# Kernel optimization log

Hardware: AMD Instinct MI355X
Metric: run time of the kernel (lower is better)

## Reference

```python
import jax, jax.numpy as jnp
import numpy as np

CONF_THRESHOLD = 0.7

def setup_inputs() -> dict:
    key = jax.random.key(0)
    ks = jax.random.split(key, 8)
    B, T, D, H, GH = 16384, 48, 32, 1024, 128
    s = lambda fan: 1.0 / np.sqrt(fan)
    return {
        "x":   jax.random.normal(ks[0], (B, T, D), jnp.float32),
        "gW1": jax.random.normal(ks[1], (D, GH), jnp.float32) * s(D),
        "gb1": jnp.zeros((GH,), jnp.float32),
        "gW2": jax.random.normal(ks[2], (GH, 2), jnp.float32) * s(GH),
        "gb2": jnp.zeros((2,), jnp.float32),
        "nW1": jax.random.normal(ks[3], (T * D, H), jnp.float32) * s(T * D),
        "nb1": jnp.zeros((H,), jnp.float32),
        "nW2": jax.random.normal(ks[4], (H, 2), jnp.float32) * s(H),
        "nb2": jnp.zeros((2,), jnp.float32),
        "aW1": jax.random.normal(ks[5], (T * D, H), jnp.float32) * s(T * D),
        "ab1": jnp.zeros((H,), jnp.float32),
        "aW2": jax.random.normal(ks[6], (H, 2), jnp.float32) * s(H),
        "ab2": jnp.zeros((2,), jnp.float32),
    }

def _gate(x, gW1, gb1, gW2, gb2):
    # mean-pool over time, 2-layer MLP, softmax -> [B, 2] class probs
    h = jax.nn.relu(jnp.mean(x, axis=1) @ gW1 + gb1)
    return jax.nn.softmax(h @ gW2 + gb2, axis=-1)

def _expert(x_flat, W1, b1, W2, b2):
    return jax.nn.relu(x_flat @ W1 + b1) @ W2 + b2

def reference(x, gW1, gb1, gW2, gb2, nW1, nb1, nW2, nb2, aW1, ab1, aW2, ab2):
    B = x.shape[0]
    gate_outputs = _gate(x, gW1, gb1, gW2, gb2)          # [B, 2]
    gate_probs = jnp.max(gate_outputs, axis=1)           # [B]
    gate_decisions = jnp.argmax(gate_outputs, axis=1)    # [B] in {0,1}

    # adaptive routing: low-confidence samples fall back to the normal expert
    high_conf = gate_probs >= CONF_THRESHOLD
    abnormal_mask = high_conf & (gate_decisions == 1)
    # normal_mask = (high_conf & dec==0) | ~high_conf  == ~abnormal_mask (partition)

    x_flat = x.reshape(B, -1)
    normal_out = _expert(x_flat, nW1, nb1, nW2, nb2)     # [B, 2]
    abnormal_out = _expert(x_flat, aW1, ab1, aW2, ab2)   # [B, 2]
    outputs = jnp.where(abnormal_mask[:, None], abnormal_out, normal_out)
    return outputs, gate_decisions, gate_probs
```

## Files before the change

kernel.cpp:

```cpp
#include <hip/hip_runtime.h>

#define TDIM 48
#define DDIM 32
#define KDIM 1536
#define HDIM 1024
#define GHID 128

typedef unsigned short u16;
typedef __bf16 bf16x8 __attribute__((ext_vector_type(8)));
typedef float  f32x4  __attribute__((ext_vector_type(4)));

typedef const void __attribute__((address_space(1))) gvoid;
typedef void       __attribute__((address_space(3))) lvoid;

__device__ __forceinline__ void gld_lds16(const void* g, void* l) {
    __builtin_amdgcn_global_load_lds((gvoid*)g, (lvoid*)l, 16, 0, 0);
}

__device__ __forceinline__ u16 f2bf(float f) {
    union { float f; unsigned u; } v; v.f = f;
    return (u16)((v.u + 0x7fffu + ((v.u >> 16) & 1u)) >> 16);
}

__global__ __launch_bounds__(256) void gate_kernel(
    const float* __restrict__ x,
    const float* __restrict__ gW1, const float* __restrict__ gb1,
    const float* __restrict__ gW2, const float* __restrict__ gb2,
    u16* __restrict__ Xbf, int* __restrict__ route, int* __restrict__ cnt,
    float* __restrict__ out, float* __restrict__ outDec, float* __restrict__ outProb)
{
    const int wave = threadIdx.x >> 6;
    const int lane = threadIdx.x & 63;
    const int b    = blockIdx.x * 4 + wave;
    if (blockIdx.x == 0 && threadIdx.x < 2) cnt[threadIdx.x] = 0;

    const float* xr = x + (size_t)b * KDIM;
    u16* xo = Xbf + (size_t)b * KDIM;

    double a0 = 0, a1 = 0, a2 = 0, a3 = 0;
#pragma unroll
    for (int i = 0; i < 6; ++i) {
        const int idx = i * 256 + lane * 4;
        float4 v = *(const float4*)(xr + idx);
        ushort4 o;
        o.x = f2bf(v.x); o.y = f2bf(v.y); o.z = f2bf(v.z); o.w = f2bf(v.w);
        *(ushort4*)(xo + idx) = o;
        a0 += v.x; a1 += v.y; a2 += v.z; a3 += v.w;
    }
#pragma unroll
    for (int m = 8; m <= 32; m <<= 1) {
        a0 += __shfl_xor(a0, m); a1 += __shfl_xor(a1, m);
        a2 += __shfl_xor(a2, m); a3 += __shfl_xor(a3, m);
    }
    __shared__ double xm[4][DDIM];
    if (lane < 8) {
        xm[wave][4 * lane + 0] = a0 / 48.0; xm[wave][4 * lane + 1] = a1 / 48.0;
        xm[wave][4 * lane + 2] = a2 / 48.0; xm[wave][4 * lane + 3] = a3 / 48.0;
    }
    __builtin_amdgcn_wave_barrier();
    __builtin_amdgcn_s_waitcnt(0);
    __threadfence_block();

    double h0 = (double)gb1[lane], h1 = (double)gb1[lane + 64];
#pragma unroll
    for (int d = 0; d < DDIM; ++d) {
        const double xv = xm[wave][d];
        h0 += xv * (double)gW1[d * GHID + lane];
        h1 += xv * (double)gW1[d * GHID + 64 + lane];
    }
    h0 = h0 > 0.0 ? h0 : 0.0;
    h1 = h1 > 0.0 ? h1 : 0.0;
    double z0 = h0 * (double)gW2[lane * 2 + 0] + h1 * (double)gW2[(lane + 64) * 2 + 0];
    double z1 = h0 * (double)gW2[lane * 2 + 1] + h1 * (double)gW2[(lane + 64) * 2 + 1];
#pragma unroll
    for (int m = 1; m <= 32; m <<= 1) {
        z0 += __shfl_xor(z0, m);
        z1 += __shfl_xor(z1, m);
    }
    if (lane == 0) {
        z0 += (double)gb2[0]; z1 += (double)gb2[1];
        const int dec = (z1 > z0) ? 1 : 0;
        const double mz = z0 > z1 ? z0 : z1;
        const double e0 = exp(z0 - mz), e1 = exp(z1 - mz);
        const double p = (e0 > e1 ? e0 : e1) / (e0 + e1);
        const float pf = (float)p;
        outDec[b]  = (float)dec;
        outProb[b] = pf;
        out[2 * b + 0] = 0.f;
        out[2 * b + 1] = 0.f;
        const int high = ((double)pf >= 0.7) ? 1 : 0;
        route[b] = (high && dec) ? 1 : 0;
    }
}

__global__ __launch_bounds__(256) void transpose_cast(
    const float* __restrict__ nW1, const float* __restrict__ aW1,
    u16* __restrict__ W1t)
{
    __shared__ float tile[32][33];
    const int e  = blockIdx.z;
    const float* W = e ? aW1 : nW1;
    u16* Wt = W1t + (size_t)e * HDIM * KDIM;
    const int bx = blockIdx.x;
    const int by = blockIdx.y;
    const int tx = threadIdx.x;
    const int ty = threadIdx.y;
#pragma unroll
    for (int r = 0; r < 32; r += 8)
        tile[ty + r][tx] = W[(size_t)(by * 32 + ty + r) * HDIM + bx * 32 + tx];
    __syncthreads();
#pragma unroll
    for (int r = 0; r < 32; r += 8)
        Wt[(size_t)(bx * 32 + ty + r) * KDIM + by * 32 + tx] = f2bf(tile[tx][ty + r]);
}

__global__ __launch_bounds__(256) void compact_kernel(
    const int* __restrict__ route, int* __restrict__ perm, int* __restrict__ cnt,
    int Bn)
{
    const int b    = blockIdx.x * 256 + threadIdx.x;
    const int lane = threadIdx.x & 63;
    const int active = (b < Bn);
    const int e = active ? route[b] : 0;
    const unsigned long long m1 = __ballot(active && e == 1);
    const unsigned long long m0 = __ballot(active && e == 0);
    const unsigned long long below = (lane == 63) ? ~0ull >> 1 : ((1ull << lane) - 1);
    int base0 = 0, base1 = 0;
    if (lane == 0) {
        if (m0) base0 = atomicAdd(&cnt[0], (int)__popcll(m0));
        if (m1) base1 = atomicAdd(&cnt[1], (int)__popcll(m1));
    }
    base0 = __shfl(base0, 0);
    base1 = __shfl(base1, 0);
    if (active) {
        const int pos = e ? base1 + (int)__popcll(m1 & below)
                          : base0 + (int)__popcll(m0 & below);
        perm[e * Bn + pos] = b;
    }
}

__global__ __launch_bounds__(256, 2) void expert_gemm(
    const u16* __restrict__ Xbf, const u16* __restrict__ W1t,
    const float* __restrict__ nb1, const float* __restrict__ nW2,
    const float* __restrict__ nb2,
    const float* __restrict__ ab1, const float* __restrict__ aW2,
    const float* __restrict__ ab2,
    const int* __restrict__ perm, const int* __restrict__ cnt,
    float* __restrict__ out, int Bn, int mBlocks)
{
    __shared__ __align__(16) u16 Alds[128 * 32];
    __shared__ __align__(16) u16 Blds[128 * 32];
    __shared__ int   permLds[128];
    __shared__ float w2Lds[128 * 2];
    __shared__ float b1Lds[128];

    const int tid = threadIdx.x;
    const int f    = (int)blockIdx.x;
    const int g    = f >> 6;
    const int nIdx = (f >> 3) & 7;
    const int mGlb = g * 8 + (f & 7);
    const int e  = mGlb >= mBlocks;
    const int mb = mGlb - (e ? mBlocks : 0);
    const int cntE = cnt[e];
    const int start = mb * 128;
    if (start >= cntE) return;
    const int valid = min(128, cntE - start);

    const int n0 = nIdx * 128;
    const u16*  W1e = W1t + (size_t)e * HDIM * KDIM;
    const float* b1 = e ? ab1 : nb1;
    const float* w2 = e ? aW2 : nW2;
    const float* b2 = e ? ab2 : nb2;

    if (tid < 128) permLds[tid] = perm[e * Bn + min(start + tid, cntE - 1)];
    if (tid >= 128) {
        const int j = tid - 128;
        b1Lds[j]        = b1[n0 + j];
        w2Lds[j * 2 + 0] = w2[(n0 + j) * 2 + 0];
        w2Lds[j * 2 + 1] = w2[(n0 + j) * 2 + 1];
    }
    __syncthreads();

    const int rA0 = permLds[tid >> 2];
    const int rA1 = permLds[(tid + 256) >> 2];
    const u16* gA0 = Xbf + (size_t)rA0 * KDIM + (tid & 3) * 8;
    const u16* gA1 = Xbf + (size_t)rA1 * KDIM + (tid & 3) * 8;
    const u16* gB0 = W1e + (size_t)(n0 + (tid >> 2)) * KDIM + (tid & 3) * 8;
    const u16* gB1 = W1e + (size_t)(n0 + 64 + (tid >> 2)) * KDIM + (tid & 3) * 8;

    const int wave = tid >> 6;
    const int lane = tid & 63;
    const int wm   = (wave & 1) * 64;
    const int wn   = (wave >> 1) * 64;
    const int l15  = lane & 15;
    const int quad = lane >> 4;

    f32x4 acc[4][4];
#pragma unroll
    for (int i = 0; i < 4; ++i)
#pragma unroll
        for (int j = 0; j < 4; ++j) acc[i][j] = (f32x4)0.f;

    for (int k0 = 0; k0 < KDIM; k0 += 32) {
        gld_lds16(gA0 + k0, &Alds[tid * 8]);
        gld_lds16(gA1 + k0, &Alds[(tid + 256) * 8]);
        gld_lds16(gB0 + k0, &Blds[tid * 8]);
        gld_lds16(gB1 + k0, &Blds[(tid + 256) * 8]);
        __syncthreads();

        bf16x8 af[4], bfv[4];
#pragma unroll
        for (int mi = 0; mi < 4; ++mi)
            af[mi] = *reinterpret_cast<const bf16x8*>(&Alds[(wm + mi * 16 + l15) * 32 + quad * 8]);
#pragma unroll
        for (int ni = 0; ni < 4; ++ni)
            bfv[ni] = *reinterpret_cast<const bf16x8*>(&Blds[(wn + ni * 16 + l15) * 32 + quad * 8]);
#pragma unroll
        for (int mi = 0; mi < 4; ++mi)
#pragma unroll
            for (int ni = 0; ni < 4; ++ni)
                acc[mi][ni] = __builtin_amdgcn_mfma_f32_16x16x32_bf16(af[mi], bfv[ni], acc[mi][ni], 0, 0, 0);
        __syncthreads();
    }

    const float b2_0 = (n0 == 0) ? b2[0] : 0.f;
    const float b2_1 = (n0 == 0) ? b2[1] : 0.f;
#pragma unroll
    for (int mi = 0; mi < 4; ++mi) {
        float p0[4] = {0.f, 0.f, 0.f, 0.f};
        float p1[4] = {0.f, 0.f, 0.f, 0.f};
#pragma unroll
        for (int ni = 0; ni < 4; ++ni) {
            const int col = wn + ni * 16 + l15;
            const float w20 = w2Lds[col * 2 + 0];
            const float w21 = w2Lds[col * 2 + 1];
            const float bb  = b1Lds[col];
#pragma unroll
            for (int r = 0; r < 4; ++r) {
                float h = acc[mi][ni][r] + bb;
                h = fmaxf(h, 0.f);
                p0[r] += h * w20;
                p1[r] += h * w21;
            }
        }
#pragma unroll
        for (int m = 1; m <= 8; m <<= 1) {
#pragma unroll
            for (int r = 0; r < 4; ++r) {
                p0[r] += __shfl_xor(p0[r], m);
                p1[r] += __shfl_xor(p1[r], m);
            }
        }
        if (l15 < 4) {
            const int r = l15;
            const int lrow = wm + mi * 16 + quad * 4 + r;
            if (lrow < valid) {
                const int srow = permLds[lrow];
                atomicAdd(&out[srow * 2 + 0], p0[r] + b2_0);
                atomicAdd(&out[srow * 2 + 1], p1[r] + b2_1);
            }
        }
    }
}

extern "C" void kernel_launch(void* const* d_in, const int* in_sizes, int n_in,
                              void* d_out, int out_size, void* d_ws, size_t ws_size,
                              hipStream_t stream) {
    const float* x   = (const float*)d_in[0];
    const float* gW1 = (const float*)d_in[1];
    const float* gb1 = (const float*)d_in[2];
    const float* gW2 = (const float*)d_in[3];
    const float* gb2 = (const float*)d_in[4];
    const float* nW1 = (const float*)d_in[5];
    const float* nb1 = (const float*)d_in[6];
    const float* nW2 = (const float*)d_in[7];
    const float* nb2 = (const float*)d_in[8];
    const float* aW1 = (const float*)d_in[9];
    const float* ab1 = (const float*)d_in[10];
    const float* aW2 = (const float*)d_in[11];
    const float* ab2 = (const float*)d_in[12];

    float* out = (float*)d_out;
    const int Bn = in_sizes[0] / KDIM;

    char* ws = (char*)d_ws;
    size_t off = 0;
    u16* Xbf = (u16*)(ws + off); off += (size_t)Bn * KDIM * sizeof(u16);
    u16* W1t = (u16*)(ws + off); off += (size_t)2 * HDIM * KDIM * sizeof(u16);
    int* perm = (int*)(ws + off); off += (size_t)2 * Bn * sizeof(int);
    int* cnt  = (int*)(ws + off); off += 2 * sizeof(int);
    int* route = (int*)(ws + off); off += (size_t)Bn * sizeof(int);

    gate_kernel<<<Bn / 4, 256, 0, stream>>>(x, gW1, gb1, gW2, gb2,
                                            Xbf, route, cnt,
                                            out, out + 2 * Bn, out + 3 * Bn);

    transpose_cast<<<dim3(HDIM / 32, KDIM / 32, 2), dim3(32, 8), 0, stream>>>(nW1, aW1, W1t);

    compact_kernel<<<(Bn + 255) / 256, 256, 0, stream>>>(route, perm, cnt, Bn);

    const int mBlocks = (Bn + 127) / 128;
    expert_gemm<<<8 * 2 * mBlocks, 256, 0, stream>>>(
        Xbf, W1t, nb1, nW2, nb2, ab1, aW2, ab2, perm, cnt, out, Bn, mBlocks);
}
```

Measured before the change: 253.8 us.

## Switch expert GEMM to 32x32x16 MFMA with K=64 tiles and k-group LDS layout

Replaces the 16x16x32 MFMA tiling with 32x32x16 bf16 MFMAs, doubles the K step per iteration to 64, and reorganizes LDS as [kgroup][row][8] so each async load fills a contiguous 16-byte slot. The aim is fewer barriers per K, fewer LDS fragment reads per FLOP, and better LDS bank behavior. The launch bound is raised to 4 blocks per CU for more occupancy. The epilogue is adapted to the 32x32 accumulator layout with a wider shuffle reduction. The higher block count may cap registers per thread and cause spills.

```diff
diff --git a/kernel.cpp b/kernel.cpp
--- a/kernel.cpp
+++ b/kernel.cpp
@@ -9,6 +9,7 @@
 typedef unsigned short u16;
 typedef __bf16 bf16x8 __attribute__((ext_vector_type(8)));
 typedef float  f32x4  __attribute__((ext_vector_type(4)));
+typedef float  f32x16 __attribute__((ext_vector_type(16)));
 
 typedef const void __attribute__((address_space(1))) gvoid;
 typedef void       __attribute__((address_space(3))) lvoid;
@@ -139,7 +140,7 @@
     }
 }
 
-__global__ __launch_bounds__(256, 2) void expert_gemm(
+__global__ __launch_bounds__(256, 4) void expert_gemm(
     const u16* __restrict__ Xbf, const u16* __restrict__ W1t,
     const float* __restrict__ nb1, const float* __restrict__ nW2,
     const float* __restrict__ nb2,
@@ -148,17 +149,17 @@
     const int* __restrict__ perm, const int* __restrict__ cnt,
     float* __restrict__ out, int Bn, int mBlocks)
 {
-    __shared__ __align__(16) u16 Alds[128 * 32];
-    __shared__ __align__(16) u16 Blds[128 * 32];
+    __shared__ __align__(16) u16 Alds[8][128][8];
+    __shared__ __align__(16) u16 Blds[8][128][8];
     __shared__ int   permLds[128];
     __shared__ float w2Lds[128 * 2];
     __shared__ float b1Lds[128];
 
     const int tid = threadIdx.x;
     const int f    = (int)blockIdx.x;
-    const int g    = f >> 6;
+    const int g4   = f >> 6;
     const int nIdx = (f >> 3) & 7;
-    const int mGlb = g * 8 + (f & 7);
+    const int mGlb = g4 * 8 + (f & 7);
     const int e  = mGlb >= mBlocks;
     const int mb = mGlb - (e ? mBlocks : 0);
     const int cntE = cnt[e];
@@ -181,83 +182,87 @@
     }
     __syncthreads();
 
-    const int rA0 = permLds[tid >> 2];
-    const int rA1 = permLds[(tid + 256) >> 2];
-    const u16* gA0 = Xbf + (size_t)rA0 * KDIM + (tid & 3) * 8;
-    const u16* gA1 = Xbf + (size_t)rA1 * KDIM + (tid & 3) * 8;
-    const u16* gB0 = W1e + (size_t)(n0 + (tid >> 2)) * KDIM + (tid & 3) * 8;
-    const u16* gB1 = W1e + (size_t)(n0 + 64 + (tid >> 2)) * KDIM + (tid & 3) * 8;
+    const int rowS  = tid & 127;
+    const int gBase = tid >> 7;
+    const u16* gA = Xbf + (size_t)permLds[rowS] * KDIM + gBase * 8;
+    const u16* gB = W1e + (size_t)(n0 + rowS) * KDIM + gBase * 8;
+    u16* la = (u16*)Alds + tid * 8;
+    u16* lb = (u16*)Blds + tid * 8;
 
     const int wave = tid >> 6;
     const int lane = tid & 63;
     const int wm   = (wave & 1) * 64;
     const int wn   = (wave >> 1) * 64;
-    const int l15  = lane & 15;
-    const int quad = lane >> 4;
-
-    f32x4 acc[4][4];
-#pragma unroll
-    for (int i = 0; i < 4; ++i)
-#pragma unroll
-        for (int j = 0; j < 4; ++j) acc[i][j] = (f32x4)0.f;
-
-    for (int k0 = 0; k0 < KDIM; k0 += 32) {
-        gld_lds16(gA0 + k0, &Alds[tid * 8]);
-        gld_lds16(gA1 + k0, &Alds[(tid + 256) * 8]);
-        gld_lds16(gB0 + k0, &Blds[tid * 8]);
-        gld_lds16(gB1 + k0, &Blds[(tid + 256) * 8]);
+    const int l31  = lane & 31;
+    const int khalf = lane >> 5;
+
+    f32x16 acc00 = (f32x16)0.f, acc01 = (f32x16)0.f;
+    f32x16 acc10 = (f32x16)0.f, acc11 = (f32x16)0.f;
+
+    for (int k0 = 0; k0 < KDIM; k0 += 64) {
+#pragma unroll
+        for (int j = 0; j < 4; ++j)
+            gld_lds16(gA + k0 + j * 16, la + j * 2048);
+#pragma unroll
+        for (int j = 0; j < 4; ++j)
+            gld_lds16(gB + k0 + j * 16, lb + j * 2048);
         __syncthreads();
 
-        bf16x8 af[4], bfv[4];
-#pragma unroll
-        for (int mi = 0; mi < 4; ++mi)
-            af[mi] = *reinterpret_cast<const bf16x8*>(&Alds[(wm + mi * 16 + l15) * 32 + quad * 8]);
-#pragma unroll
-        for (int ni = 0; ni < 4; ++ni)
-            bfv[ni] = *reinterpret_cast<const bf16x8*>(&Blds[(wn + ni * 16 + l15) * 32 + quad * 8]);
-#pragma unroll
-        for (int mi = 0; mi < 4; ++mi)
-#pragma unroll
-            for (int ni = 0; ni < 4; ++ni)
-                acc[mi][ni] = __builtin_amdgcn_mfma_f32_16x16x32_bf16(af[mi], bfv[ni], acc[mi][ni], 0, 0, 0);
+#pragma unroll
+        for (int t = 0; t < 4; ++t) {
+            const int g = 2 * t + khalf;
+            bf16x8 af0 = *reinterpret_cast<const bf16x8*>(&Alds[g][wm + l31][0]);
+            bf16x8 af1 = *reinterpret_cast<const bf16x8*>(&Alds[g][wm + 32 + l31][0]);
+            bf16x8 bv0 = *reinterpret_cast<const bf16x8*>(&Blds[g][wn + l31][0]);
+            bf16x8 bv1 = *reinterpret_cast<const bf16x8*>(&Blds[g][wn + 32 + l31][0]);
+            acc00 = __builtin_amdgcn_mfma_f32_32x32x16_bf16(af0, bv0, acc00, 0, 0, 0);
+            acc01 = __builtin_amdgcn_mfma_f32_32x32x16_bf16(af0, bv1, acc01, 0, 0, 0);
+            acc10 = __builtin_amdgcn_mfma_f32_32x32x16_bf16(af1, bv0, acc10, 0, 0, 0);
+            acc11 = __builtin_amdgcn_mfma_f32_32x32x16_bf16(af1, bv1, acc11, 0, 0, 0);
+        }
         __syncthreads();
     }
 
     const float b2_0 = (n0 == 0) ? b2[0] : 0.f;
     const float b2_1 = (n0 == 0) ? b2[1] : 0.f;
 #pragma unroll
-    for (int mi = 0; mi < 4; ++mi) {
-        float p0[4] = {0.f, 0.f, 0.f, 0.f};
-        float p1[4] = {0.f, 0.f, 0.f, 0.f};
-#pragma unroll
-        for (int ni = 0; ni < 4; ++ni) {
-            const int col = wn + ni * 16 + l15;
+    for (int mi = 0; mi < 2; ++mi) {
+        float p0[16], p1[16];
+#pragma unroll
+        for (int r = 0; r < 16; ++r) { p0[r] = 0.f; p1[r] = 0.f; }
+#pragma unroll
+        for (int ni = 0; ni < 2; ++ni) {
+            const f32x16 a = (mi == 0) ? (ni == 0 ? acc00 : acc01)
+                                       : (ni == 0 ? acc10 : acc11);
+            const int col = wn + ni * 32 + l31;
             const float w20 = w2Lds[col * 2 + 0];
             const float w21 = w2Lds[col * 2 + 1];
             const float bb  = b1Lds[col];
 #pragma unroll
-            for (int r = 0; r < 4; ++r) {
-                float h = acc[mi][ni][r] + bb;
+            for (int r = 0; r < 16; ++r) {
+                float h = a[r] + bb;
                 h = fmaxf(h, 0.f);
                 p0[r] += h * w20;
                 p1[r] += h * w21;
             }
         }
 #pragma unroll
-        for (int m = 1; m <= 8; m <<= 1) {
-#pragma unroll
-            for (int r = 0; r < 4; ++r) {
+        for (int m = 1; m <= 16; m <<= 1) {
+#pragma unroll
+            for (int r = 0; r < 16; ++r) {
                 p0[r] += __shfl_xor(p0[r], m);
                 p1[r] += __shfl_xor(p1[r], m);
             }
         }
-        if (l15 < 4) {
-            const int r = l15;
-            const int lrow = wm + mi * 16 + quad * 4 + r;
-            if (lrow < valid) {
-                const int srow = permLds[lrow];
-                atomicAdd(&out[srow * 2 + 0], p0[r] + b2_0);
-                atomicAdd(&out[srow * 2 + 1], p1[r] + b2_1);
+        if (l31 == 0) {
+#pragma unroll
+            for (int r = 0; r < 16; ++r) {
+                const int lrow = wm + mi * 32 + (r & 3) + 8 * (r >> 2) + 4 * khalf;
+                if (lrow < valid) {
+                    const int srow = permLds[lrow];
+                    atomicAdd(&out[srow * 2 + 0], p0[r] + b2_0);
+                    atomicAdd(&out[srow * 2 + 1], p1[r] + b2_1);
+                }
             }
         }
     }
```

Result: slower. 328.8 us (+29.6%).

## Double K-tile to 64 with XOR-swizzled LDS layout in expert GEMM

Applied to the files above, without the earlier changes.

The K step per loop iteration grows from 32 to 64, so each block stages a 128x64 A and B tile and runs two MFMA sub-steps between barriers, halving the number of __syncthreads per GEMM. Global-to-LDS loads now map 8 threads per row and XOR-swizzle the 16-byte column chunk by row index, and the fragment reads apply the same swizzle, so LDS reads with a 128-byte row stride should avoid bank conflicts. LDS use doubles to about 32KB per block, which may limit occupancy at two blocks per CU. There is still no double buffering, so load latency stays exposed at each barrier.

```diff
diff --git a/kernel.cpp b/kernel.cpp
--- a/kernel.cpp
+++ b/kernel.cpp
@@ -148,17 +148,17 @@
     const int* __restrict__ perm, const int* __restrict__ cnt,
     float* __restrict__ out, int Bn, int mBlocks)
 {
-    __shared__ __align__(16) u16 Alds[128 * 32];
-    __shared__ __align__(16) u16 Blds[128 * 32];
+    __shared__ __align__(16) u16 Alds[128 * 64];
+    __shared__ __align__(16) u16 Blds[128 * 64];
     __shared__ int   permLds[128];
     __shared__ float w2Lds[128 * 2];
     __shared__ float b1Lds[128];
 
     const int tid = threadIdx.x;
     const int f    = (int)blockIdx.x;
-    const int g    = f >> 6;
+    const int g4   = f >> 6;
     const int nIdx = (f >> 3) & 7;
-    const int mGlb = g * 8 + (f & 7);
+    const int mGlb = g4 * 8 + (f & 7);
     const int e  = mGlb >= mBlocks;
     const int mb = mGlb - (e ? mBlocks : 0);
     const int cntE = cnt[e];
@@ -181,12 +181,16 @@
     }
     __syncthreads();
 
-    const int rA0 = permLds[tid >> 2];
-    const int rA1 = permLds[(tid + 256) >> 2];
-    const u16* gA0 = Xbf + (size_t)rA0 * KDIM + (tid & 3) * 8;
-    const u16* gA1 = Xbf + (size_t)rA1 * KDIM + (tid & 3) * 8;
-    const u16* gB0 = W1e + (size_t)(n0 + (tid >> 2)) * KDIM + (tid & 3) * 8;
-    const u16* gB1 = W1e + (size_t)(n0 + 64 + (tid >> 2)) * KDIM + (tid & 3) * 8;
+    const int rbase = tid >> 3;
+    const int cg    = (tid & 7) ^ (rbase & 7);
+    const u16* gA[4]; const u16* gB[4];
+#pragma unroll
+    for (int j = 0; j < 4; ++j) {
+        gA[j] = Xbf + (size_t)permLds[rbase + 32 * j] * KDIM + cg * 8;
+        gB[j] = W1e + (size_t)(n0 + rbase + 32 * j) * KDIM + cg * 8;
+    }
+    u16* la = (u16*)Alds + tid * 8;
+    u16* lb = (u16*)Blds + tid * 8;
 
     const int wave = tid >> 6;
     const int lane = tid & 63;
@@ -201,25 +205,36 @@
 #pragma unroll
         for (int j = 0; j < 4; ++j) acc[i][j] = (f32x4)0.f;
 
-    for (int k0 = 0; k0 < KDIM; k0 += 32) {
-        gld_lds16(gA0 + k0, &Alds[tid * 8]);
-        gld_lds16(gA1 + k0, &Alds[(tid + 256) * 8]);
-        gld_lds16(gB0 + k0, &Blds[tid * 8]);
-        gld_lds16(gB1 + k0, &Blds[(tid + 256) * 8]);
+    for (int k0 = 0; k0 < KDIM; k0 += 64) {
+#pragma unroll
+        for (int j = 0; j < 4; ++j)
+            gld_lds16(gA[j] + k0, la + j * 2048);
+#pragma unroll
+        for (int j = 0; j < 4; ++j)
+            gld_lds16(gB[j] + k0, lb + j * 2048);
         __syncthreads();
 
-        bf16x8 af[4], bfv[4];
-#pragma unroll
-        for (int mi = 0; mi < 4; ++mi)
-            af[mi] = *reinterpret_cast<const bf16x8*>(&Alds[(wm + mi * 16 + l15) * 32 + quad * 8]);
-#pragma unroll
-        for (int ni = 0; ni < 4; ++ni)
-            bfv[ni] = *reinterpret_cast<const bf16x8*>(&Blds[(wn + ni * 16 + l15) * 32 + quad * 8]);
-#pragma unroll
-        for (int mi = 0; mi < 4; ++mi)
-#pragma unroll
-            for (int ni = 0; ni < 4; ++ni)
-                acc[mi][ni] = __builtin_amdgcn_mfma_f32_16x16x32_bf16(af[mi], bfv[ni], acc[mi][ni], 0, 0, 0);
+#pragma unroll
+        for (int t = 0; t < 2; ++t) {
+            bf16x8 af[4], bfv[4];
+#pragma unroll
+            for (int mi = 0; mi < 4; ++mi) {
+                const int r = wm + mi * 16 + l15;
+                const int p = (t * 4 + quad) ^ (r & 7);
+                af[mi] = *reinterpret_cast<const bf16x8*>(&Alds[r * 64 + p * 8]);
+            }
+#pragma unroll
+            for (int ni = 0; ni < 4; ++ni) {
+                const int r = wn + ni * 16 + l15;
+                const int p = (t * 4 + quad) ^ (r & 7);
+                bfv[ni] = *reinterpret_cast<const bf16x8*>(&Blds[r * 64 + p * 8]);
+            }
+#pragma unroll
+            for (int mi = 0; mi < 4; ++mi)
+#pragma unroll
+                for (int ni = 0; ni < 4; ++ni)
+                    acc[mi][ni] = __builtin_amdgcn_mfma_f32_16x16x32_bf16(af[mi], bfv[ni], acc[mi][ni], 0, 0, 0);
+        }
         __syncthreads();
     }
 
```

New measurement: 247.6 us. -2.4%, faster.
